# Kernel optimization log

Measured on AMD Instinct MI355X. Metric: run time of the kernel, lower is better.

## Reference

```python
import jax, jax.numpy as jnp
import numpy as np

B, T, D_IN, H, D_OUT = 256, 2048, 128, 128, 128


def setup_inputs() -> dict:
    key = jax.random.key(0)
    ks = jax.random.split(key, 7)
    s_in = 1.0 / np.sqrt(H)
    return {
        "x": jax.random.normal(ks[0], (B, T, D_IN), dtype=jnp.float32),
        "Wih": jax.random.normal(ks[1], (4 * H, D_IN), dtype=jnp.float32) * s_in,
        "Whh": jax.random.normal(ks[2], (4 * H, H), dtype=jnp.float32) * s_in,
        "bih": jax.random.normal(ks[3], (4 * H,), dtype=jnp.float32) * s_in,
        "bhh": jax.random.normal(ks[4], (4 * H,), dtype=jnp.float32) * s_in,
        "Wo": jax.random.normal(ks[5], (D_OUT, H), dtype=jnp.float32) * s_in,
        "bo": jax.random.normal(ks[6], (D_OUT,), dtype=jnp.float32) * s_in,
    }


def reference(x, Wih, Whh, bih, bhh, Wo, bo):
    # LSTM recurrence over time; module returns only the last step's
    # output projection (outputs[:, -1, :]).
    batch, seq_len, _ = x.shape
    h0 = jnp.zeros((batch, Whh.shape[1]), dtype=x.dtype)
    c0 = jnp.zeros_like(h0)
    # Precompute input-side gate projections for all timesteps in one GEMM.
    xg = jnp.einsum('btd,gd->btg', x, Wih) + bih + bhh  # [B, T, 4H]
    xg = jnp.swapaxes(xg, 0, 1)  # [T, B, 4H] for scan

    def step(carry, xg_t):
        h, c = carry
        gates = xg_t + h @ Whh.T  # [B, 4H]
        i, f, g, o = jnp.split(gates, 4, axis=-1)
        i = jax.nn.sigmoid(i)
        f = jax.nn.sigmoid(f)
        g = jnp.tanh(g)
        o = jax.nn.sigmoid(o)
        c = f * c + i * g
        h = o * jnp.tanh(c)
        return (h, c), None

    (h_last, _), _ = jax.lax.scan(step, (h0, c0), xg)
    return h_last @ Wo.T + bo  # [B, D_OUT]
```

## Files before the change

kernel.cpp:

```cpp
#include <hip/hip_runtime.h>
#include <hip/hip_fp16.h>

#define B_  256
#define T_  2048
#define D_  128
#define H_  128
#define G_  512
#define CH  32
#define NCH (T_ / CH)

typedef __attribute__((ext_vector_type(8))) short    short8;
typedef __attribute__((ext_vector_type(4))) float    floatx4;
typedef __attribute__((ext_vector_type(2))) _Float16 half2v;

static __device__ __forceinline__ unsigned pack_bf16(float a, float b) {
  unsigned ua = __builtin_bit_cast(unsigned, a);
  unsigned ub = __builtin_bit_cast(unsigned, b);
  ua = ua + 0x7fffu + ((ua >> 16) & 1u);
  ub = ub + 0x7fffu + ((ub >> 16) & 1u);
  return (ua >> 16) | (ub & 0xffff0000u);
}

static __device__ __forceinline__ float fdot2f(unsigned w, unsigned h, float acc) {
  return __builtin_amdgcn_fdot2(__builtin_bit_cast(half2v, w),
                                __builtin_bit_cast(half2v, h), acc, false);
}

static __device__ __forceinline__ float sigm_fast(float x) {
  float e = __builtin_amdgcn_exp2f(x * -1.44269504088896341f);
  return __builtin_amdgcn_rcpf(1.0f + e);
}
static __device__ __forceinline__ float tanh_fast(float x) {
  float e = __builtin_amdgcn_exp2f(x * 2.88539008177792681f);
  return 1.0f - 2.0f * __builtin_amdgcn_rcpf(e + 1.0f);
}

#define QBCAST(v, pat)                                                         \
  __builtin_bit_cast(float, __builtin_amdgcn_mov_dpp(                          \
      __builtin_bit_cast(int, v), (pat), 0xF, 0xF, false))

__global__ __launch_bounds__(512, 2) void lstm_fused(
    const float* __restrict__ x,   const float* __restrict__ Wih,
    const float* __restrict__ Whh, const float* __restrict__ bih,
    const float* __restrict__ bhh, const float* __restrict__ Wo,
    const float* __restrict__ bo,  float* __restrict__ out)
{
  __shared__ unsigned       xs[CH][68];
  __shared__ unsigned short xgb[CH][G_];
  __shared__ __align__(16) unsigned hbuf[2][64];

  const int tid  = threadIdx.x;
  const int b    = blockIdx.x;
  const int lane = tid & 63;
  const int wv   = tid >> 6;
  const int q    = tid & 3;
  const int j    = tid >> 2;
  const int grow = q * H_ + j;
  const int quad = lane >> 4;
  const int m16  = lane & 15;

  unsigned wpk[64];
  {
    const float2* wr = (const float2*)(Whh + (size_t)grow * H_);
    #pragma unroll
    for (int k = 0; k < 64; ++k) {
      float2 v = wr[k];
      wpk[k] = __builtin_bit_cast(unsigned, __builtin_amdgcn_cvt_pkrtz(v.x, v.y));
    }
  }
  const float bias = bih[grow] + bhh[grow];

  uint4 bfr[4][4];
  #pragma unroll
  for (int nt = 0; nt < 4; ++nt) {
    int row = wv * 64 + nt * 16 + m16;
    const float4* p = (const float4*)(Wih + (size_t)row * D_);
    #pragma unroll
    for (int kf = 0; kf < 4; ++kf) {
      float4 f0 = p[kf * 8 + quad * 2];
      float4 f1 = p[kf * 8 + quad * 2 + 1];
      uint4 u;
      u.x = pack_bf16(f0.x, f0.y);  u.y = pack_bf16(f0.z, f0.w);
      u.z = pack_bf16(f1.x, f1.y);  u.w = pack_bf16(f1.z, f1.w);
      bfr[nt][kf] = u;
    }
  }

  if (tid < 64) { hbuf[0][tid] = 0u; hbuf[1][tid] = 0u; }
  float c = 0.0f;
  __syncthreads();

  const float* xb = x + (size_t)b * T_ * D_;

  for (int ch = 0; ch < NCH; ++ch) {
    const float4* xsrc = (const float4*)(xb + (size_t)ch * CH * D_);
    #pragma unroll
    for (int i = 0; i < 2; ++i) {
      int fi = i * 512 + tid;
      float4 v = xsrc[fi];
      int t  = fi >> 5;
      int kp = (fi & 31) * 2;
      xs[t][kp]     = pack_bf16(v.x, v.y);
      xs[t][kp + 1] = pack_bf16(v.z, v.w);
    }
    __syncthreads();

    #pragma unroll
    for (int mt = 0; mt < 2; ++mt) {
      short8 af[4];
      #pragma unroll
      for (int kf = 0; kf < 4; ++kf) {
        const uint4* ap = (const uint4*)&xs[mt * 16 + m16][kf * 16 + quad * 4];
        af[kf] = __builtin_bit_cast(short8, *ap);
      }
      #pragma unroll
      for (int nt = 0; nt < 4; ++nt) {
        floatx4 acc = {0.f, 0.f, 0.f, 0.f};
        #pragma unroll
        for (int kf = 0; kf < 4; ++kf)
          acc = __builtin_amdgcn_mfma_f32_16x16x32_bf16(
              af[kf], __builtin_bit_cast(short8, bfr[nt][kf]), acc, 0, 0, 0);
        int gcol = wv * 64 + nt * 16 + m16;
        int pg   = (gcol & 127) * 4 + (gcol >> 7);
        #pragma unroll
        for (int r = 0; r < 4; ++r) {
          int trow = mt * 16 + quad * 4 + r;
          xgb[trow][pg] = __half_as_ushort(__float2half(acc[r]));
        }
      }
    }
    __syncthreads();

    for (int tt = 0; tt < CH; ++tt) {
      const uint4* hb4 = (const uint4*)hbuf[tt & 1];
      float a0 = bias + __half2float(__ushort_as_half(xgb[tt][tid]));
      float a1 = 0.f, a2 = 0.f, a3 = 0.f;
      #pragma unroll
      for (int jj = 0; jj < 16; ++jj) {
        uint4 hv = hb4[jj];
        a0 = fdot2f(wpk[4 * jj + 0], hv.x, a0);
        a1 = fdot2f(wpk[4 * jj + 1], hv.y, a1);
        a2 = fdot2f(wpk[4 * jj + 2], hv.z, a2);
        a3 = fdot2f(wpk[4 * jj + 3], hv.w, a3);
      }
      float gate = (a0 + a1) + (a2 + a3);
      float av = (q == 2) ? tanh_fast(gate) : sigm_fast(gate);
      float gi = QBCAST(av, 0x00);
      float gf = QBCAST(av, 0x55);
      float gg = QBCAST(av, 0xAA);
      float go = QBCAST(av, 0xFF);
      c = gf * c + gi * gg;
      float h = go * tanh_fast(c);
      if (q == 0)
        ((unsigned short*)hbuf[(tt & 1) ^ 1])[j] = __half_as_ushort(__float2half(h));
      __syncthreads();
    }
  }

  if (tid < H_) {
    float acc = bo[tid];
    const float4* wr = (const float4*)(Wo + (size_t)tid * H_);
    const uint2* hp = (const uint2*)hbuf[0];
    #pragma unroll
    for (int k4 = 0; k4 < 32; ++k4) {
      float4 w  = wr[k4];
      uint2  hu = hp[k4];
      half2v h01 = __builtin_bit_cast(half2v, hu.x);
      half2v h23 = __builtin_bit_cast(half2v, hu.y);
      acc += w.x * (float)h01[0] + w.y * (float)h01[1]
           + w.z * (float)h23[0] + w.w * (float)h23[1];
    }
    out[(size_t)b * H_ + tid] = acc;
  }
}

extern "C" void kernel_launch(void* const* d_in, const int* in_sizes, int n_in,
                              void* d_out, int out_size, void* d_ws, size_t ws_size,
                              hipStream_t stream) {
  (void)in_sizes; (void)n_in; (void)d_ws; (void)ws_size; (void)out_size;
  const float* x   = (const float*)d_in[0];
  const float* Wih = (const float*)d_in[1];
  const float* Whh = (const float*)d_in[2];
  const float* bih = (const float*)d_in[3];
  const float* bhh = (const float*)d_in[4];
  const float* Wo  = (const float*)d_in[5];
  const float* bo  = (const float*)d_in[6];
  lstm_fused<<<B_, 512, 0, stream>>>(x, Wih, Whh, bih, bhh, Wo, bo, (float*)d_out);
}
```

Baseline: 1.460 ms.

## Compute recurrent h@Whh with MFMA instead of per-thread fdot2 loops

```diff
diff --git a/kernel.cpp b/kernel.cpp
--- a/kernel.cpp
+++ b/kernel.cpp
@@ -5,88 +5,81 @@
 #define T_  2048
 #define D_  128
 #define H_  128
-#define G_  512
 #define CH  32
 #define NCH (T_ / CH)
 
-typedef __attribute__((ext_vector_type(8))) short    short8;
+#define NLOG2E  (-1.4426950408889634f)
+#define LOG2E2  ( 2.8853900817779268f)
+
+typedef __attribute__((ext_vector_type(8))) _Float16 half8v;
 typedef __attribute__((ext_vector_type(4))) float    floatx4;
-typedef __attribute__((ext_vector_type(2))) _Float16 half2v;
 
-static __device__ __forceinline__ unsigned pack_bf16(float a, float b) {
-  unsigned ua = __builtin_bit_cast(unsigned, a);
-  unsigned ub = __builtin_bit_cast(unsigned, b);
-  ua = ua + 0x7fffu + ((ua >> 16) & 1u);
-  ub = ub + 0x7fffu + ((ub >> 16) & 1u);
-  return (ua >> 16) | (ub & 0xffff0000u);
+static __device__ __forceinline__ unsigned pkh(float a, float b) {
+  return __builtin_bit_cast(unsigned, __builtin_amdgcn_cvt_pkrtz(a, b));
 }
+static __device__ __forceinline__ float h2f_lo(unsigned u) {
+  return __half2float(__ushort_as_half((unsigned short)(u & 0xffffu)));
+}
+static __device__ __forceinline__ float h2f_hi(unsigned u) {
+  return __half2float(__ushort_as_half((unsigned short)(u >> 16)));
+}
+#define SEL4(v, n) (((n) & 2) ? (((n) & 1) ? (v)[3] : (v)[2]) \
+                              : (((n) & 1) ? (v)[1] : (v)[0]))
 
-static __device__ __forceinline__ float fdot2f(unsigned w, unsigned h, float acc) {
-  return __builtin_amdgcn_fdot2(__builtin_bit_cast(half2v, w),
-                                __builtin_bit_cast(half2v, h), acc, false);
-}
-
-static __device__ __forceinline__ float sigm_fast(float x) {
-  float e = __builtin_amdgcn_exp2f(x * -1.44269504088896341f);
-  return __builtin_amdgcn_rcpf(1.0f + e);
-}
-static __device__ __forceinline__ float tanh_fast(float x) {
-  float e = __builtin_amdgcn_exp2f(x * 2.88539008177792681f);
-  return 1.0f - 2.0f * __builtin_amdgcn_rcpf(e + 1.0f);
-}
-
-#define QBCAST(v, pat)                                                         \
-  __builtin_bit_cast(float, __builtin_amdgcn_mov_dpp(                          \
-      __builtin_bit_cast(int, v), (pat), 0xF, 0xF, false))
-
-__global__ __launch_bounds__(512, 2) void lstm_fused(
+__global__ __launch_bounds__(512, 2) void lstm_mfma(
     const float* __restrict__ x,   const float* __restrict__ Wih,
     const float* __restrict__ Whh, const float* __restrict__ bih,
     const float* __restrict__ bhh, const float* __restrict__ Wo,
     const float* __restrict__ bo,  float* __restrict__ out)
 {
   __shared__ unsigned       xs[CH][68];
-  __shared__ unsigned short xgb[CH][G_];
+  __shared__ unsigned short xgf[CH][4 * H_];
   __shared__ __align__(16) unsigned hbuf[2][64];
 
   const int tid  = threadIdx.x;
   const int b    = blockIdx.x;
   const int lane = tid & 63;
   const int wv   = tid >> 6;
-  const int q    = tid & 3;
-  const int j    = tid >> 2;
-  const int grow = q * H_ + j;
   const int quad = lane >> 4;
   const int m16  = lane & 15;
 
-  unsigned wpk[64];
-  {
-    const float2* wr = (const float2*)(Whh + (size_t)grow * H_);
-    #pragma unroll
-    for (int k = 0; k < 64; ++k) {
-      float2 v = wr[k];
-      wpk[k] = __builtin_bit_cast(unsigned, __builtin_amdgcn_cvt_pkrtz(v.x, v.y));
-    }
-  }
-  const float bias = bih[grow] + bhh[grow];
-
-  uint4 bfr[4][4];
+  uint4 wa[4][4];
   #pragma unroll
-  for (int nt = 0; nt < 4; ++nt) {
-    int row = wv * 64 + nt * 16 + m16;
-    const float4* p = (const float4*)(Wih + (size_t)row * D_);
+  for (int mt = 0; mt < 4; ++mt) {
+    float s = (mt == 2) ? LOG2E2 : NLOG2E;
+    const float4* p = (const float4*)(Whh + (size_t)(mt * 128 + wv * 16 + m16) * H_);
     #pragma unroll
     for (int kf = 0; kf < 4; ++kf) {
       float4 f0 = p[kf * 8 + quad * 2];
       float4 f1 = p[kf * 8 + quad * 2 + 1];
       uint4 u;
-      u.x = pack_bf16(f0.x, f0.y);  u.y = pack_bf16(f0.z, f0.w);
-      u.z = pack_bf16(f1.x, f1.y);  u.w = pack_bf16(f1.z, f1.w);
-      bfr[nt][kf] = u;
+      u.x = pkh(f0.x * s, f0.y * s);  u.y = pkh(f0.z * s, f0.w * s);
+      u.z = pkh(f1.x * s, f1.y * s);  u.w = pkh(f1.z * s, f1.w * s);
+      wa[mt][kf] = u;
     }
   }
 
-  if (tid < 64) { hbuf[0][tid] = 0u; hbuf[1][tid] = 0u; }
+  const float sW = ((wv >> 1) == 2) ? LOG2E2 : NLOG2E;
+  uint4 wb[4][4];
+  float bv[4];
+  #pragma unroll
+  for (int nt = 0; nt < 4; ++nt) {
+    int gcol = wv * 64 + nt * 16 + m16;
+    const float4* p = (const float4*)(Wih + (size_t)gcol * D_);
+    #pragma unroll
+    for (int kf = 0; kf < 4; ++kf) {
+      float4 f0 = p[kf * 8 + quad * 2];
+      float4 f1 = p[kf * 8 + quad * 2 + 1];
+      uint4 u;
+      u.x = pkh(f0.x * sW, f0.y * sW);  u.y = pkh(f0.z * sW, f0.w * sW);
+      u.z = pkh(f1.x * sW, f1.y * sW);  u.w = pkh(f1.z * sW, f1.w * sW);
+      wb[nt][kf] = u;
+    }
+    bv[nt] = (bih[gcol] + bhh[gcol]) * sW;
+  }
+
+  if (tid < 128) hbuf[tid >> 6][tid & 63] = 0u;
+  uint4 hfr[4] = {{0,0,0,0},{0,0,0,0},{0,0,0,0},{0,0,0,0}};
   float c = 0.0f;
   __syncthreads();
 
@@ -100,59 +93,77 @@
       float4 v = xsrc[fi];
       int t  = fi >> 5;
       int kp = (fi & 31) * 2;
-      xs[t][kp]     = pack_bf16(v.x, v.y);
-      xs[t][kp + 1] = pack_bf16(v.z, v.w);
+      xs[t][kp]     = pkh(v.x, v.y);
+      xs[t][kp + 1] = pkh(v.z, v.w);
     }
     __syncthreads();
 
     #pragma unroll
     for (int mt = 0; mt < 2; ++mt) {
-      short8 af[4];
+      half8v af[4];
       #pragma unroll
-      for (int kf = 0; kf < 4; ++kf) {
-        const uint4* ap = (const uint4*)&xs[mt * 16 + m16][kf * 16 + quad * 4];
-        af[kf] = __builtin_bit_cast(short8, *ap);
-      }
+      for (int kf = 0; kf < 4; ++kf)
+        af[kf] = __builtin_bit_cast(half8v,
+                   *(const uint4*)&xs[mt * 16 + m16][kf * 16 + quad * 4]);
       #pragma unroll
       for (int nt = 0; nt < 4; ++nt) {
         floatx4 acc = {0.f, 0.f, 0.f, 0.f};
         #pragma unroll
         for (int kf = 0; kf < 4; ++kf)
-          acc = __builtin_amdgcn_mfma_f32_16x16x32_bf16(
-              af[kf], __builtin_bit_cast(short8, bfr[nt][kf]), acc, 0, 0, 0);
+          acc = __builtin_amdgcn_mfma_f32_16x16x32_f16(
+              af[kf], __builtin_bit_cast(half8v, wb[nt][kf]), acc, 0, 0, 0);
         int gcol = wv * 64 + nt * 16 + m16;
-        int pg   = (gcol & 127) * 4 + (gcol >> 7);
+        int jc   = gcol & 127, gt = gcol >> 7;
         #pragma unroll
         for (int r = 0; r < 4; ++r) {
           int trow = mt * 16 + quad * 4 + r;
-          xgb[trow][pg] = __half_as_ushort(__float2half(acc[r]));
+          xgf[trow][jc * 4 + gt] =
+              __half_as_ushort(__float2half(acc[r] + bv[nt]));
         }
       }
     }
     __syncthreads();
 
     for (int tt = 0; tt < CH; ++tt) {
-      const uint4* hb4 = (const uint4*)hbuf[tt & 1];
-      float a0 = bias + __half2float(__ushort_as_half(xgb[tt][tid]));
-      float a1 = 0.f, a2 = 0.f, a3 = 0.f;
+      const int rp = (ch * CH + tt) & 1;
+      unsigned long long xv = 0ull;
+      if (m16 < 4) {
+        xv = *(const unsigned long long*)&xgf[tt][(wv * 16 + quad * 4 + m16) * 4];
+        #pragma unroll
+        for (int kf = 0; kf < 4; ++kf)
+          hfr[kf] = *(const uint4*)&hbuf[rp][kf * 16 + quad * 4];
+      }
+      floatx4 a0 = {0,0,0,0}, a1 = {0,0,0,0}, a2 = {0,0,0,0}, a3 = {0,0,0,0};
       #pragma unroll
-      for (int jj = 0; jj < 16; ++jj) {
-        uint4 hv = hb4[jj];
-        a0 = fdot2f(wpk[4 * jj + 0], hv.x, a0);
-        a1 = fdot2f(wpk[4 * jj + 1], hv.y, a1);
-        a2 = fdot2f(wpk[4 * jj + 2], hv.z, a2);
-        a3 = fdot2f(wpk[4 * jj + 3], hv.w, a3);
+      for (int kf = 0; kf < 4; ++kf) {
+        half8v hb = __builtin_bit_cast(half8v, hfr[kf]);
+        a0 = __builtin_amdgcn_mfma_f32_16x16x32_f16(
+                 __builtin_bit_cast(half8v, wa[0][kf]), hb, a0, 0, 0, 0);
+        a1 = __builtin_amdgcn_mfma_f32_16x16x32_f16(
+                 __builtin_bit_cast(half8v, wa[1][kf]), hb, a1, 0, 0, 0);
+        a2 = __builtin_amdgcn_mfma_f32_16x16x32_f16(
+                 __builtin_bit_cast(half8v, wa[2][kf]), hb, a2, 0, 0, 0);
+        a3 = __builtin_amdgcn_mfma_f32_16x16x32_f16(
+                 __builtin_bit_cast(half8v, wa[3][kf]), hb, a3, 0, 0, 0);
       }
-      float gate = (a0 + a1) + (a2 + a3);
-      float av = (q == 2) ? tanh_fast(gate) : sigm_fast(gate);
-      float gi = QBCAST(av, 0x00);
-      float gf = QBCAST(av, 0x55);
-      float gg = QBCAST(av, 0xAA);
-      float go = QBCAST(av, 0xFF);
-      c = gf * c + gi * gg;
-      float h = go * tanh_fast(c);
-      if (q == 0)
-        ((unsigned short*)hbuf[(tt & 1) ^ 1])[j] = __half_as_ushort(__float2half(h));
+      if (m16 < 4) {
+        const int n = m16;
+        const int j = wv * 16 + quad * 4 + n;
+        unsigned xlo = (unsigned)xv, xhi = (unsigned)(xv >> 32);
+        float pi = SEL4(a0, n) + h2f_lo(xlo);
+        float pf = SEL4(a1, n) + h2f_hi(xlo);
+        float pg = SEL4(a2, n) + h2f_lo(xhi);
+        float po = SEL4(a3, n) + h2f_hi(xhi);
+        float gi = __builtin_amdgcn_rcpf(1.0f + __builtin_amdgcn_exp2f(pi));
+        float gf = __builtin_amdgcn_rcpf(1.0f + __builtin_amdgcn_exp2f(pf));
+        float go = __builtin_amdgcn_rcpf(1.0f + __builtin_amdgcn_exp2f(po));
+        float gg = 1.0f - 2.0f * __builtin_amdgcn_rcpf(1.0f + __builtin_amdgcn_exp2f(pg));
+        c = gf * c + gi * gg;
+        float tc = 1.0f - 2.0f * __builtin_amdgcn_rcpf(
+                       1.0f + __builtin_amdgcn_exp2f(c * LOG2E2));
+        float h = go * tc;
+        ((unsigned short*)hbuf[rp ^ 1])[j] = __half_as_ushort(__float2half(h));
+      }
       __syncthreads();
     }
   }
@@ -165,10 +176,8 @@
     for (int k4 = 0; k4 < 32; ++k4) {
       float4 w  = wr[k4];
       uint2  hu = hp[k4];
-      half2v h01 = __builtin_bit_cast(half2v, hu.x);
-      half2v h23 = __builtin_bit_cast(half2v, hu.y);
-      acc += w.x * (float)h01[0] + w.y * (float)h01[1]
-           + w.z * (float)h23[0] + w.w * (float)h23[1];
+      acc += w.x * h2f_lo(hu.x) + w.y * h2f_hi(hu.x)
+           + w.z * h2f_lo(hu.y) + w.w * h2f_hi(hu.y);
     }
     out[(size_t)b * H_ + tid] = acc;
   }
@@ -185,5 +194,5 @@
   const float* bhh = (const float*)d_in[4];
   const float* Wo  = (const float*)d_in[5];
   const float* bo  = (const float*)d_in[6];
-  lstm_fused<<<B_, 512, 0, stream>>>(x, Wih, Whh, bih, bhh, Wo, bo, (float*)d_out);
+  lstm_mfma<<<B_, 512, 0, stream>>>(x, Wih, Whh, bih, bhh, Wo, bo, (float*)d_out);
 }
```

After: 1.315 ms. 9.9% less time.
